# Performance work log

Hardware: AMD Instinct MI355X
Metric: run time of the kernel (lower is better)

## Reference

```python
import jax, jax.numpy as jnp
import numpy as np

N_NODES = 50000
N_EDGES = 800000


def _gcn_conv(x, W, b, src, dst, norm, n_nodes):
    # PyG GCNConv: out = D^{-1/2} (A + I) D^{-1/2} (x W) + b
    h = x @ W                                  # [N, out]
    msg = h[src] * norm[:, None]               # [E+N, out] gathered, normalized messages
    agg = jax.ops.segment_sum(msg, dst, num_segments=n_nodes)
    return agg + b


def _build_norm(edge_index, n_nodes):
    # add self-loops, compute symmetric degree normalization
    loop = jnp.arange(n_nodes, dtype=edge_index.dtype)
    src = jnp.concatenate([edge_index[0], loop])
    dst = jnp.concatenate([edge_index[1], loop])
    deg = jnp.zeros((n_nodes,), jnp.float32).at[dst].add(1.0)
    dinv = jnp.where(deg > 0, jax.lax.rsqrt(deg), 0.0)
    norm = dinv[src] * dinv[dst]
    return src, dst, norm


def setup_inputs() -> dict:
    key = jax.random.key(0)
    ks = jax.random.split(key, 5)
    x = jax.random.normal(ks[0], (N_NODES, 128), dtype=jnp.float32)
    edge_index = jax.random.randint(ks[1], (2, N_EDGES), 0, N_NODES, dtype=jnp.int64)
    s1 = 1.0 / np.sqrt(128)
    s2 = 1.0 / np.sqrt(128)
    s3 = 1.0 / np.sqrt(64)
    return {
        "x": x,
        "edge_index": edge_index,
        "W1": jax.random.normal(ks[2], (128, 128), dtype=jnp.float32) * s1,
        "b1": jnp.zeros((128,), jnp.float32),
        "W2": jax.random.normal(ks[3], (128, 64), dtype=jnp.float32) * s2,
        "b2": jnp.zeros((64,), jnp.float32),
        "W3": jax.random.normal(ks[4], (64, 128), dtype=jnp.float32) * s3,
        "b3": jnp.zeros((128,), jnp.float32),
    }


def reference(x, edge_index, W1, b1, W2, b2, W3, b3):
    n = x.shape[0]
    src, dst, norm = _build_norm(edge_index, n)
    # dropout is identity in eval mode
    h = jax.nn.relu(_gcn_conv(x, W1, b1, src, dst, norm, n))
    h = jax.nn.relu(_gcn_conv(h, W2, b2, src, dst, norm, n))
    out = _gcn_conv(h, W3, b3, src, dst, norm, n)
    return out
```

## Files before the change

### kernel.cpp

```cpp
#include <hip/hip_runtime.h>


#define DEV_INLINE __device__ __forceinline__

typedef unsigned int uint;
typedef unsigned short ushort;
typedef __attribute__((ext_vector_type(8))) short bf16x8;
typedef __attribute__((ext_vector_type(4))) float f32x4;

static DEV_INLINE uint f2bf_rne(float f) {
    uint u = __float_as_uint(f);
    return (u + 0x7FFFu + ((u >> 16) & 1u)) >> 16;
}
static DEV_INLINE uint pack2(float a, float b) { return f2bf_rne(a) | (f2bf_rne(b) << 16); }
static DEV_INLINE float bflo(uint u) { return __uint_as_float(u << 16); }
static DEV_INLINE float bfhi(uint u) { return __uint_as_float(u & 0xFFFF0000u); }

static DEV_INLINE void fma8(float4& a, float4& b, float n, const uint4& v) {
    a.x = fmaf(n, bflo(v.x), a.x); a.y = fmaf(n, bfhi(v.x), a.y);
    a.z = fmaf(n, bflo(v.y), a.z); a.w = fmaf(n, bfhi(v.y), a.w);
    b.x = fmaf(n, bflo(v.z), b.x); b.y = fmaf(n, bfhi(v.z), b.y);
    b.z = fmaf(n, bflo(v.w), b.z); b.w = fmaf(n, bfhi(v.w), b.w);
}

static DEV_INLINE void split8(const float4& x0, const float4& x1, bf16x8& ah, bf16x8& al) {
    float xs[8] = {x0.x, x0.y, x0.z, x0.w, x1.x, x1.y, x1.z, x1.w};
#pragma unroll
    for (int j = 0; j < 8; ++j) {
        uint u = __float_as_uint(xs[j]);
        ah[j] = (short)(u >> 16);
        float r = xs[j] - __uint_as_float(u & 0xFFFF0000u);
        al[j] = (short)(__float_as_uint(r) >> 16);
    }
}


__global__ __launch_bounds__(256) void hist_coarse_kernel(
    const int* __restrict__ dst, int* __restrict__ cnt196, int E, int NBK)
{
    __shared__ int h[256];
    if ((int)threadIdx.x < NBK) h[threadIdx.x] = 0;
    __syncthreads();
    for (int i = blockIdx.x * blockDim.x + threadIdx.x; i < E; i += gridDim.x * blockDim.x)
        atomicAdd(&h[dst[i] >> 8], 1);
    __syncthreads();
    if ((int)threadIdx.x < NBK) {
        int v = h[threadIdx.x];
        if (v) atomicAdd(&cnt196[threadIdx.x], v);
    }
}

__global__ void scan_coarse_kernel(const int* __restrict__ cnt196, int* __restrict__ base196,
                                   int* __restrict__ cursor196, int* __restrict__ rowptr,
                                   int NBK, int N, int E)
{
    __shared__ int buf[256];
    const int tid = threadIdx.x;
    int v = (tid < NBK) ? cnt196[tid] : 0;
    buf[tid] = v;
    __syncthreads();
#pragma unroll
    for (int ofs = 1; ofs < 256; ofs <<= 1) {
        int t = (tid >= ofs) ? buf[tid - ofs] : 0;
        __syncthreads();
        buf[tid] += t;
        __syncthreads();
    }
    if (tid < NBK) {
        int b = buf[tid] - v;
        base196[tid] = b;
        cursor196[tid] = b;
    }
    if (tid == 0) rowptr[N] = E;
}

__global__ __launch_bounds__(256) void scatter_coarse_kernel(
    const int* __restrict__ src, const int* __restrict__ dst,
    int* __restrict__ cursor196, uint* __restrict__ pkg, int E, int NBK)
{
    __shared__ int histL[256];
    __shared__ int baseL[256];
    const int tid = threadIdx.x;
    const int c0  = blockIdx.x * 2048;
    if (tid < NBK) histL[tid] = 0;
    __syncthreads();

    uint mypk[8];
    int  myn = 0;
#pragma unroll
    for (int k = 0; k < 8; ++k) {
        int idx = c0 + k * 256 + tid;
        if (idx < E) {
            uint pk = ((uint)dst[idx] << 16) | (uint)(src[idx] & 0xFFFF);
            mypk[myn++] = pk;
            atomicAdd(&histL[pk >> 24], 1);
        }
    }
    __syncthreads();
    if (tid < NBK) {
        int h = histL[tid];
        baseL[tid] = (h > 0) ? atomicAdd(&cursor196[tid], h) : 0;
        histL[tid] = 0;
    }
    __syncthreads();
    for (int k = 0; k < myn; ++k) {
        uint pk = mypk[k];
        int b = pk >> 24;
        int pos = baseL[b] + atomicAdd(&histL[b], 1);
        pkg[pos] = pk;
    }
}

__global__ __launch_bounds__(256) void build_fine_kernel(
    const uint* __restrict__ pkg, const int* __restrict__ cnt196,
    const int* __restrict__ base196, int* __restrict__ rowptr,
    float* __restrict__ dinv, ushort* __restrict__ perm, int N)
{
    __shared__ uint   pkL[8192];
    __shared__ ushort outS[8192];
    __shared__ int hist[256];
    __shared__ int buf[256];
    const int b   = blockIdx.x;
    const int tid = threadIdx.x;
    const int base = base196[b];
    int nE = cnt196[b];
    if (nE > 8192) nE = 8192;

    hist[tid] = 0;
    __syncthreads();
    for (int i = tid; i < nE; i += 256) {
        uint pk = pkg[base + i];
        pkL[i] = pk;
        atomicAdd(&hist[(pk >> 16) & 255], 1);
    }
    __syncthreads();

    int cnt = hist[tid];
    buf[tid] = cnt;
    __syncthreads();
#pragma unroll
    for (int ofs = 1; ofs < 256; ofs <<= 1) {
        int t = (tid >= ofs) ? buf[tid - ofs] : 0;
        __syncthreads();
        buf[tid] += t;
        __syncthreads();
    }
    int excl = buf[tid] - cnt;
    int node = b * 256 + tid;
    if (node < N) {
        rowptr[node] = base + excl;
        dinv[node]   = rsqrtf((float)(cnt + 1));
    }
    hist[tid] = excl;
    __syncthreads();
    for (int i = tid; i < nE; i += 256) {
        uint pk = pkL[i];
        int d = (pk >> 16) & 255;
        int pos = atomicAdd(&hist[d], 1);
        outS[pos] = (ushort)(pk & 0xFFFFu);
    }
    __syncthreads();
    for (int i = tid; i < nE; i += 256) perm[base + i] = outS[i];
}


template<int K, int NOUT>
static DEV_INLINE void prep_one(const float* __restrict__ W,
                                ushort* __restrict__ Wh, ushort* __restrict__ Wl, int id) {
    constexpr int C = NOUT / 16;
    int lane = id & 63;
    int tc   = id >> 6;
    int c = tc % C, t = tc / C;
    int krow = t * 32 + (lane >> 4) * 8;
    int col  = c * 16 + (lane & 15);
#pragma unroll
    for (int j = 0; j < 8; ++j) {
        float w = W[(size_t)(krow + j) * NOUT + col];
        uint u = __float_as_uint(w);
        Wh[(size_t)id * 8 + j] = (ushort)(u >> 16);
        float r = w - __uint_as_float(u & 0xFFFF0000u);
        Wl[(size_t)id * 8 + j] = (ushort)(__float_as_uint(r) >> 16);
    }
}

__global__ void prep_wfrag_all_kernel(
    const float* __restrict__ W1, const float* __restrict__ W2, const float* __restrict__ W3,
    ushort* w1h, ushort* w1l, ushort* w2h, ushort* w2l, ushort* w3h, ushort* w3l)
{
    int id = blockIdx.x * 256 + threadIdx.x;
    if (id < 2048)       prep_one<128, 128>(W1, w1h, w1l, id);
    else if (id < 3072)  prep_one<128, 64>(W2, w2h, w2l, id - 2048);
    else if (id < 4096)  prep_one<64, 128>(W3, w3h, w3l, id - 3072);
}


template<int K, int NOUT, bool ABF, bool PRE, bool POSTB, bool OUTBF>
__global__ __launch_bounds__(256) void gemm_mfma_kernel(
    const void* __restrict__ A, const ushort* __restrict__ Whf, const ushort* __restrict__ Wlf,
    const float* __restrict__ bias_k, const float* __restrict__ bias_n,
    void* __restrict__ Cout, int N)
{
    constexpr int C  = NOUT / 16;
    constexpr int T  = K / 32;
    const int tid  = threadIdx.x;
    const int w    = tid >> 6;
    const int lane = tid & 63;
    const int row0 = blockIdx.x * 64 + w * 16;

    const int arow  = row0 + (lane & 15);
    const int arowc = (arow < N) ? arow : (N - 1);
    const int lq    = (lane >> 4);

    const bf16x8* WH = reinterpret_cast<const bf16x8*>(Whf);
    const bf16x8* WL = reinterpret_cast<const bf16x8*>(Wlf);

    f32x4 acc[C];
#pragma unroll
    for (int c = 0; c < C; ++c) acc[c] = (f32x4){0.f, 0.f, 0.f, 0.f};

#pragma unroll
    for (int t = 0; t < T; ++t) {
        bf16x8 ah, al;
        if (ABF) {
            const ushort* ap = (const ushort*)A + (size_t)arowc * K + t * 32 + lq * 8;
            ah = *reinterpret_cast<const bf16x8*>(ap);
        } else {
            const float* ap = (const float*)A + (size_t)arowc * K + t * 32 + lq * 8;
            float4 x0 = *reinterpret_cast<const float4*>(ap);
            float4 x1 = *reinterpret_cast<const float4*>(ap + 4);
            if (PRE) {
                const float* bp = bias_k + t * 32 + lq * 8;
                float4 b0 = *reinterpret_cast<const float4*>(bp);
                float4 b1 = *reinterpret_cast<const float4*>(bp + 4);
                x0.x = fmaxf(x0.x + b0.x, 0.f); x0.y = fmaxf(x0.y + b0.y, 0.f);
                x0.z = fmaxf(x0.z + b0.z, 0.f); x0.w = fmaxf(x0.w + b0.w, 0.f);
                x1.x = fmaxf(x1.x + b1.x, 0.f); x1.y = fmaxf(x1.y + b1.y, 0.f);
                x1.z = fmaxf(x1.z + b1.z, 0.f); x1.w = fmaxf(x1.w + b1.w, 0.f);
            }
            split8(x0, x1, ah, al);
        }
#pragma unroll
        for (int c = 0; c < C; ++c) {
            bf16x8 bh = WH[(t * C + c) * 64 + lane];
            bf16x8 bl = WL[(t * C + c) * 64 + lane];
            acc[c] = __builtin_amdgcn_mfma_f32_16x16x32_bf16(ah, bh, acc[c], 0, 0, 0);
            if (!ABF)
                acc[c] = __builtin_amdgcn_mfma_f32_16x16x32_bf16(al, bh, acc[c], 0, 0, 0);
            acc[c] = __builtin_amdgcn_mfma_f32_16x16x32_bf16(ah, bl, acc[c], 0, 0, 0);
        }
    }

    const int rbase = (lane >> 4) * 4;
    const int ccol  = (lane & 15);
#pragma unroll
    for (int c = 0; c < C; ++c) {
        int col = c * 16 + ccol;
        float pb = POSTB ? bias_n[col] : 0.f;
#pragma unroll
        for (int r = 0; r < 4; ++r) {
            int row = row0 + rbase + r;
            if (row < N) {
                float v = acc[c][r] + pb;
                if (OUTBF) ((ushort*)Cout)[(size_t)row * NOUT + col] = (ushort)f2bf_rne(v);
                else       ((float*)Cout)[(size_t)row * NOUT + col] = v;
            }
        }
    }
}


template<int F, bool BIAS, bool RELU, bool OUTBF>
__global__ __launch_bounds__(256) void agg_gather_kernel(
    const uint* __restrict__ H, const int* __restrict__ rowptr,
    const ushort* __restrict__ perm_src, const float* __restrict__ dinv,
    const float* __restrict__ bias, void* __restrict__ OUT, int N)
{
    constexpr int GROUP = F / 8;
    constexpr int FW    = F / 2;
    constexpr int NPB   = 256 / GROUP;
    const int lane = threadIdx.x % GROUP;
    const int g    = threadIdx.x / GROUP;
    const int node = blockIdx.x * NPB + g;
    if (node >= N) return;

    const int beg = rowptr[node];
    const int end = rowptr[node + 1];
    const float di = dinv[node];

    float4 aA = make_float4(0.f, 0.f, 0.f, 0.f), aB = aA;
    float4 bA = aA, bB = aA;
    {
        uint4 v = reinterpret_cast<const uint4*>(H + (size_t)node * FW)[lane];
        fma8(aA, aB, di * di, v);
    }

    int e = beg;
    for (; e + 3 < end; e += 4) {
        int s0 = perm_src[e];     int s1 = perm_src[e + 1];
        int s2 = perm_src[e + 2]; int s3 = perm_src[e + 3];
        float n0 = dinv[s0] * di, n1 = dinv[s1] * di;
        float n2 = dinv[s2] * di, n3 = dinv[s3] * di;
        uint4 v0 = reinterpret_cast<const uint4*>(H + (size_t)s0 * FW)[lane];
        uint4 v1 = reinterpret_cast<const uint4*>(H + (size_t)s1 * FW)[lane];
        uint4 v2 = reinterpret_cast<const uint4*>(H + (size_t)s2 * FW)[lane];
        uint4 v3 = reinterpret_cast<const uint4*>(H + (size_t)s3 * FW)[lane];
        fma8(aA, aB, n0, v0);
        fma8(bA, bB, n1, v1);
        fma8(aA, aB, n2, v2);
        fma8(bA, bB, n3, v3);
    }
    for (; e < end; ++e) {
        int s0 = perm_src[e];
        float n0 = dinv[s0] * di;
        uint4 v0 = reinterpret_cast<const uint4*>(H + (size_t)s0 * FW)[lane];
        fma8(aA, aB, n0, v0);
    }
    aA.x += bA.x; aA.y += bA.y; aA.z += bA.z; aA.w += bA.w;
    aB.x += bB.x; aB.y += bB.y; aB.z += bB.z; aB.w += bB.w;

    if (BIAS) {
        const float4* b4 = reinterpret_cast<const float4*>(bias);
        float4 c0 = b4[lane * 2], c1 = b4[lane * 2 + 1];
        aA.x += c0.x; aA.y += c0.y; aA.z += c0.z; aA.w += c0.w;
        aB.x += c1.x; aB.y += c1.y; aB.z += c1.z; aB.w += c1.w;
    }
    if (RELU) {
        aA.x = fmaxf(aA.x, 0.f); aA.y = fmaxf(aA.y, 0.f);
        aA.z = fmaxf(aA.z, 0.f); aA.w = fmaxf(aA.w, 0.f);
        aB.x = fmaxf(aB.x, 0.f); aB.y = fmaxf(aB.y, 0.f);
        aB.z = fmaxf(aB.z, 0.f); aB.w = fmaxf(aB.w, 0.f);
    }

    if (OUTBF) {
        uint4 u;
        u.x = pack2(aA.x, aA.y); u.y = pack2(aA.z, aA.w);
        u.z = pack2(aB.x, aB.y); u.w = pack2(aB.z, aB.w);
        reinterpret_cast<uint4*>((uint*)OUT + (size_t)node * FW)[lane] = u;
    } else {
        float4* O = reinterpret_cast<float4*>((float*)OUT + (size_t)node * F);
        O[lane * 2]     = aA;
        O[lane * 2 + 1] = aB;
    }
}


static inline size_t align_up(size_t v, size_t a) { return (v + a - 1) / a * a; }

extern "C" void kernel_launch(void* const* d_in, const int* in_sizes, int n_in,
                              void* d_out, int out_size, void* d_ws, size_t ws_size,
                              hipStream_t stream) {
    const float* x  = (const float*)d_in[0];
    const int*   ei = (const int*)d_in[1];
    const float* W1 = (const float*)d_in[2];
    const float* b1 = (const float*)d_in[3];
    const float* W2 = (const float*)d_in[4];
    const float* b2 = (const float*)d_in[5];
    const float* W3 = (const float*)d_in[6];
    const float* b3 = (const float*)d_in[7];
    float* out = (float*)d_out;

    const int N = in_sizes[0] / 128;
    const int E = in_sizes[1] / 2;
    const int* src = ei;
    const int* dst = ei + E;
    const int NBK = (N + 255) / 256;

    char* ws = (char*)d_ws;
    size_t off = 0;
    float* dinv   = (float*)(ws + off); off = align_up(off + (size_t)N * 4, 512);
    int*   rowptr = (int*)  (ws + off); off = align_up(off + (size_t)(N + 1) * 4, 512);
    int*   cnt196    = (int*)(ws + off); off = align_up(off + (size_t)NBK * 4, 512);
    int*   base196   = (int*)(ws + off); off = align_up(off + (size_t)NBK * 4, 512);
    int*   cursor196 = (int*)(ws + off); off = align_up(off + (size_t)NBK * 4, 512);
    ushort* perm_src = (ushort*)(ws + off); off = align_up(off + (size_t)E * 2, 512);
    uint*  pkg    = (uint*) (ws + off); off = align_up(off + (size_t)E * 4, 512);
    uint*  Hbf    = (uint*) (ws + off); off = align_up(off + (size_t)N * 128 * 2, 512);
    char*  Ashare = (char*) (ws + off); off = align_up(off + (size_t)N * 128 * 4, 512);
    ushort* w1h   = (ushort*)(ws + off); off = align_up(off + (size_t)128 * 128 * 2, 512);
    ushort* w1l   = (ushort*)(ws + off); off = align_up(off + (size_t)128 * 128 * 2, 512);
    ushort* w2h   = (ushort*)(ws + off); off = align_up(off + (size_t)128 * 64 * 2, 512);
    ushort* w2l   = (ushort*)(ws + off); off = align_up(off + (size_t)128 * 64 * 2, 512);
    ushort* w3h   = (ushort*)(ws + off); off = align_up(off + (size_t)64 * 128 * 2, 512);
    ushort* w3l   = (ushort*)(ws + off); off = align_up(off + (size_t)64 * 128 * 2, 512);
    (void)ws_size;

    uint* H1bf   = Hbf;
    uint* H2bf   = Hbf;
    uint* H3bf   = Hbf + (size_t)N * 32;
    uint* AGG1bf = (uint*)Ashare;
    float* T     = (float*)Ashare;

    const int TPB = 256;
    dim3 blk(TPB);
    int gRow = (N + 63) / 64;

    prep_wfrag_all_kernel<<<16, blk, 0, stream>>>(W1, W2, W3, w1h, w1l, w2h, w2l, w3h, w3l);

    hipMemsetAsync(cnt196, 0, (size_t)NBK * 4, stream);
    hist_coarse_kernel<<<392, blk, 0, stream>>>(dst, cnt196, E, NBK);
    scan_coarse_kernel<<<1, blk, 0, stream>>>(cnt196, base196, cursor196, rowptr, NBK, N, E);
    scatter_coarse_kernel<<<(E + 2047) / 2048, blk, 0, stream>>>(src, dst, cursor196, pkg, E, NBK);
    build_fine_kernel<<<NBK, blk, 0, stream>>>(pkg, cnt196, base196, rowptr, dinv, perm_src, N);

    gemm_mfma_kernel<128, 128, false, false, false, true><<<gRow, blk, 0, stream>>>(
        x, w1h, w1l, nullptr, nullptr, H1bf, N);
    agg_gather_kernel<128, true, true, true><<<(N + 15) / 16, blk, 0, stream>>>(
        H1bf, rowptr, perm_src, dinv, b1, AGG1bf, N);

    gemm_mfma_kernel<128, 64, true, false, false, true><<<gRow, blk, 0, stream>>>(
        AGG1bf, w2h, w2l, nullptr, nullptr, H2bf, N);
    agg_gather_kernel<64, true, true, true><<<(N + 31) / 32, blk, 0, stream>>>(
        H2bf, rowptr, perm_src, dinv, b2, H3bf, N);

    agg_gather_kernel<64, false, false, false><<<(N + 31) / 32, blk, 0, stream>>>(
        H3bf, rowptr, perm_src, dinv, nullptr, T, N);
    gemm_mfma_kernel<64, 128, false, false, true, false><<<gRow, blk, 0, stream>>>(
        T, w3h, w3l, nullptr, b3, out, N);
}
```

Baseline: 229.6 us.

## Fold dinv into GEMM outputs and fuse aggregation with following GEMMs

Pre-scales each GEMM output row by dinv[src] so the gather no longer loads dinv per neighbour; the aggregation becomes a plain sum and is scaled by dinv[dst] afterwards. The layer-1 aggregation is fused with the layer-2 GEMM, and the layer-3 aggregation with the layer-3 GEMM, through an LDS tile, so the float/bf16 intermediates no longer make a round trip through global memory. The scatter kernel re-reads src and dst instead of holding the packed values in registers. This cuts kernel launches and intermediate traffic, at the cost of a gather-phase load imbalance inside each fused block and a changed rounding order.

```diff
diff --git a/kernel.cpp b/kernel.cpp
--- a/kernel.cpp
+++ b/kernel.cpp
@@ -12,15 +12,14 @@
     uint u = __float_as_uint(f);
     return (u + 0x7FFFu + ((u >> 16) & 1u)) >> 16;
 }
-static DEV_INLINE uint pack2(float a, float b) { return f2bf_rne(a) | (f2bf_rne(b) << 16); }
 static DEV_INLINE float bflo(uint u) { return __uint_as_float(u << 16); }
 static DEV_INLINE float bfhi(uint u) { return __uint_as_float(u & 0xFFFF0000u); }
 
-static DEV_INLINE void fma8(float4& a, float4& b, float n, const uint4& v) {
-    a.x = fmaf(n, bflo(v.x), a.x); a.y = fmaf(n, bfhi(v.x), a.y);
-    a.z = fmaf(n, bflo(v.y), a.z); a.w = fmaf(n, bfhi(v.y), a.w);
-    b.x = fmaf(n, bflo(v.z), b.x); b.y = fmaf(n, bfhi(v.z), b.y);
-    b.z = fmaf(n, bflo(v.w), b.z); b.w = fmaf(n, bfhi(v.w), b.w);
+static DEV_INLINE void add8(float4& a, float4& b, const uint4& v) {
+    a.x += bflo(v.x); a.y += bfhi(v.x);
+    a.z += bflo(v.y); a.w += bfhi(v.y);
+    b.x += bflo(v.z); b.y += bfhi(v.z);
+    b.z += bflo(v.w); b.w += bfhi(v.w);
 }
 
 static DEV_INLINE void split8(const float4& x0, const float4& x1, bf16x8& ah, bf16x8& al) {
@@ -34,6 +33,40 @@
     }
 }
 
+template<int FW>
+static DEV_INLINE void gather_sum(const uint* __restrict__ H, const ushort* __restrict__ perm,
+                                  int beg, int end, int lane, float4& o0, float4& o1)
+{
+    float4 A0 = o0, A1 = o1;
+    float4 B0 = make_float4(0.f,0.f,0.f,0.f), B1 = B0, C0 = B0, C1 = B0, D0 = B0, D1 = B0;
+    const uint4* Hv = reinterpret_cast<const uint4*>(H);
+    int e = beg;
+    for (; e + 8 <= end; e += 8) {
+        int s0 = perm[e];     int s1 = perm[e + 1];
+        int s2 = perm[e + 2]; int s3 = perm[e + 3];
+        int s4 = perm[e + 4]; int s5 = perm[e + 5];
+        int s6 = perm[e + 6]; int s7 = perm[e + 7];
+        uint4 v0 = Hv[(size_t)s0 * (FW / 4) + lane];
+        uint4 v1 = Hv[(size_t)s1 * (FW / 4) + lane];
+        uint4 v2 = Hv[(size_t)s2 * (FW / 4) + lane];
+        uint4 v3 = Hv[(size_t)s3 * (FW / 4) + lane];
+        uint4 v4 = Hv[(size_t)s4 * (FW / 4) + lane];
+        uint4 v5 = Hv[(size_t)s5 * (FW / 4) + lane];
+        uint4 v6 = Hv[(size_t)s6 * (FW / 4) + lane];
+        uint4 v7 = Hv[(size_t)s7 * (FW / 4) + lane];
+        add8(A0, A1, v0); add8(B0, B1, v1); add8(C0, C1, v2); add8(D0, D1, v3);
+        add8(A0, A1, v4); add8(B0, B1, v5); add8(C0, C1, v6); add8(D0, D1, v7);
+    }
+    for (; e < end; ++e) {
+        uint4 v = Hv[(size_t)perm[e] * (FW / 4) + lane];
+        add8(A0, A1, v);
+    }
+    o0.x = A0.x + B0.x + C0.x + D0.x; o0.y = A0.y + B0.y + C0.y + D0.y;
+    o0.z = A0.z + B0.z + C0.z + D0.z; o0.w = A0.w + B0.w + C0.w + D0.w;
+    o1.x = A1.x + B1.x + C1.x + D1.x; o1.y = A1.y + B1.y + C1.y + D1.y;
+    o1.z = A1.z + B1.z + C1.z + D1.z; o1.w = A1.w + B1.w + C1.w + D1.w;
+}
+
 
 __global__ __launch_bounds__(256) void hist_coarse_kernel(
     const int* __restrict__ dst, int* __restrict__ cnt196, int E, int NBK)
@@ -84,17 +117,10 @@
     const int c0  = blockIdx.x * 2048;
     if (tid < NBK) histL[tid] = 0;
     __syncthreads();
-
-    uint mypk[8];
-    int  myn = 0;
 #pragma unroll
     for (int k = 0; k < 8; ++k) {
         int idx = c0 + k * 256 + tid;
-        if (idx < E) {
-            uint pk = ((uint)dst[idx] << 16) | (uint)(src[idx] & 0xFFFF);
-            mypk[myn++] = pk;
-            atomicAdd(&histL[pk >> 24], 1);
-        }
+        if (idx < E) atomicAdd(&histL[dst[idx] >> 8], 1);
     }
     __syncthreads();
     if (tid < NBK) {
@@ -103,11 +129,15 @@
         histL[tid] = 0;
     }
     __syncthreads();
-    for (int k = 0; k < myn; ++k) {
-        uint pk = mypk[k];
-        int b = pk >> 24;
-        int pos = baseL[b] + atomicAdd(&histL[b], 1);
-        pkg[pos] = pk;
+#pragma unroll
+    for (int k = 0; k < 8; ++k) {
+        int idx = c0 + k * 256 + tid;
+        if (idx < E) {
+            int d = dst[idx];
+            int b = d >> 8;
+            int pos = baseL[b] + atomicAdd(&histL[b], 1);
+            pkg[pos] = ((uint)d << 16) | (uint)(src[idx] & 0xFFFF);
+        }
     }
 }
 
@@ -194,19 +224,15 @@
 }
 
 
-template<int K, int NOUT, bool ABF, bool PRE, bool POSTB, bool OUTBF>
-__global__ __launch_bounds__(256) void gemm_mfma_kernel(
-    const void* __restrict__ A, const ushort* __restrict__ Whf, const ushort* __restrict__ Wlf,
-    const float* __restrict__ bias_k, const float* __restrict__ bias_n,
-    void* __restrict__ Cout, int N)
-{
-    constexpr int C  = NOUT / 16;
-    constexpr int T  = K / 32;
+__global__ __launch_bounds__(256) void gemm1_kernel(
+    const float* __restrict__ A, const ushort* __restrict__ Whf, const ushort* __restrict__ Wlf,
+    const float* __restrict__ dinv, ushort* __restrict__ Cout, int N)
+{
+    constexpr int C = 8, T = 4, K = 128, NOUT = 128;
     const int tid  = threadIdx.x;
     const int w    = tid >> 6;
     const int lane = tid & 63;
     const int row0 = blockIdx.x * 64 + w * 16;
-
     const int arow  = row0 + (lane & 15);
     const int arowc = (arow < N) ? arow : (N - 1);
     const int lq    = (lane >> 4);
@@ -220,32 +246,17 @@
 
 #pragma unroll
     for (int t = 0; t < T; ++t) {
+        const float* ap = A + (size_t)arowc * K + t * 32 + lq * 8;
+        float4 x0 = *reinterpret_cast<const float4*>(ap);
+        float4 x1 = *reinterpret_cast<const float4*>(ap + 4);
         bf16x8 ah, al;
-        if (ABF) {
-            const ushort* ap = (const ushort*)A + (size_t)arowc * K + t * 32 + lq * 8;
-            ah = *reinterpret_cast<const bf16x8*>(ap);
-        } else {
-            const float* ap = (const float*)A + (size_t)arowc * K + t * 32 + lq * 8;
-            float4 x0 = *reinterpret_cast<const float4*>(ap);
-            float4 x1 = *reinterpret_cast<const float4*>(ap + 4);
-            if (PRE) {
-                const float* bp = bias_k + t * 32 + lq * 8;
-                float4 b0 = *reinterpret_cast<const float4*>(bp);
-                float4 b1 = *reinterpret_cast<const float4*>(bp + 4);
-                x0.x = fmaxf(x0.x + b0.x, 0.f); x0.y = fmaxf(x0.y + b0.y, 0.f);
-                x0.z = fmaxf(x0.z + b0.z, 0.f); x0.w = fmaxf(x0.w + b0.w, 0.f);
-                x1.x = fmaxf(x1.x + b1.x, 0.f); x1.y = fmaxf(x1.y + b1.y, 0.f);
-                x1.z = fmaxf(x1.z + b1.z, 0.f); x1.w = fmaxf(x1.w + b1.w, 0.f);
-            }
-            split8(x0, x1, ah, al);
-        }
+        split8(x0, x1, ah, al);
 #pragma unroll
         for (int c = 0; c < C; ++c) {
             bf16x8 bh = WH[(t * C + c) * 64 + lane];
             bf16x8 bl = WL[(t * C + c) * 64 + lane];
             acc[c] = __builtin_amdgcn_mfma_f32_16x16x32_bf16(ah, bh, acc[c], 0, 0, 0);
-            if (!ABF)
-                acc[c] = __builtin_amdgcn_mfma_f32_16x16x32_bf16(al, bh, acc[c], 0, 0, 0);
+            acc[c] = __builtin_amdgcn_mfma_f32_16x16x32_bf16(al, bh, acc[c], 0, 0, 0);
             acc[c] = __builtin_amdgcn_mfma_f32_16x16x32_bf16(ah, bl, acc[c], 0, 0, 0);
         }
     }
@@ -253,31 +264,111 @@
     const int rbase = (lane >> 4) * 4;
     const int ccol  = (lane & 15);
 #pragma unroll
-    for (int c = 0; c < C; ++c) {
-        int col = c * 16 + ccol;
-        float pb = POSTB ? bias_n[col] : 0.f;
-#pragma unroll
-        for (int r = 0; r < 4; ++r) {
-            int row = row0 + rbase + r;
-            if (row < N) {
-                float v = acc[c][r] + pb;
-                if (OUTBF) ((ushort*)Cout)[(size_t)row * NOUT + col] = (ushort)f2bf_rne(v);
-                else       ((float*)Cout)[(size_t)row * NOUT + col] = v;
+    for (int r = 0; r < 4; ++r) {
+        int row = row0 + rbase + r;
+        if (row < N) {
+            float di = dinv[row];
+#pragma unroll
+            for (int c = 0; c < C; ++c) {
+                int col = c * 16 + ccol;
+                Cout[(size_t)row * NOUT + col] = (ushort)f2bf_rne(acc[c][r] * di);
             }
         }
     }
 }
 
 
-template<int F, bool BIAS, bool RELU, bool OUTBF>
-__global__ __launch_bounds__(256) void agg_gather_kernel(
+__global__ __launch_bounds__(256) void fused_agg1_gemm2_kernel(
+    const uint* __restrict__ H1, const int* __restrict__ rowptr,
+    const ushort* __restrict__ perm, const float* __restrict__ dinv,
+    const float* __restrict__ b1, const ushort* __restrict__ w2h,
+    const ushort* __restrict__ w2l, ushort* __restrict__ H2, int N)
+{
+    __shared__ float As[64][132];
+    const int tid  = threadIdx.x;
+    const int row0 = blockIdx.x * 64;
+
+    {
+        const int lg = tid & 15;
+        const int g  = tid >> 4;
+        const float4* b4 = reinterpret_cast<const float4*>(b1);
+        float4 bb0 = b4[lg * 2], bb1 = b4[lg * 2 + 1];
+#pragma unroll
+        for (int p = 0; p < 4; ++p) {
+            int nl = p * 16 + g;
+            int node = row0 + nl;
+            int nodec = (node < N) ? node : (N - 1);
+            int beg = rowptr[nodec], end = rowptr[nodec + 1];
+            float di = dinv[nodec];
+            float4 o0 = make_float4(0.f,0.f,0.f,0.f), o1 = o0;
+            uint4 sv = reinterpret_cast<const uint4*>(H1 + (size_t)nodec * 64)[lg];
+            add8(o0, o1, sv);
+            gather_sum<64>(H1, perm, beg, end, lg, o0, o1);
+            float4 r0, r1;
+            r0.x = fmaxf(fmaf(di, o0.x, bb0.x), 0.f);
+            r0.y = fmaxf(fmaf(di, o0.y, bb0.y), 0.f);
+            r0.z = fmaxf(fmaf(di, o0.z, bb0.z), 0.f);
+            r0.w = fmaxf(fmaf(di, o0.w, bb0.w), 0.f);
+            r1.x = fmaxf(fmaf(di, o1.x, bb1.x), 0.f);
+            r1.y = fmaxf(fmaf(di, o1.y, bb1.y), 0.f);
+            r1.z = fmaxf(fmaf(di, o1.z, bb1.z), 0.f);
+            r1.w = fmaxf(fmaf(di, o1.w, bb1.w), 0.f);
+            *reinterpret_cast<float4*>(&As[nl][lg * 8])     = r0;
+            *reinterpret_cast<float4*>(&As[nl][lg * 8 + 4]) = r1;
+        }
+    }
+    __syncthreads();
+
+    const int w    = tid >> 6;
+    const int lane = tid & 63;
+    const int ar   = w * 16 + (lane & 15);
+    const int lq   = lane >> 4;
+    const bf16x8* WH = reinterpret_cast<const bf16x8*>(w2h);
+    const bf16x8* WL = reinterpret_cast<const bf16x8*>(w2l);
+
+    f32x4 acc[4];
+#pragma unroll
+    for (int c = 0; c < 4; ++c) acc[c] = (f32x4){0.f, 0.f, 0.f, 0.f};
+
+#pragma unroll
+    for (int t = 0; t < 4; ++t) {
+        float4 x0 = *reinterpret_cast<const float4*>(&As[ar][t * 32 + lq * 8]);
+        float4 x1 = *reinterpret_cast<const float4*>(&As[ar][t * 32 + lq * 8 + 4]);
+        bf16x8 ah, al;
+        split8(x0, x1, ah, al);
+#pragma unroll
+        for (int c = 0; c < 4; ++c) {
+            bf16x8 bh = WH[(t * 4 + c) * 64 + lane];
+            bf16x8 bl = WL[(t * 4 + c) * 64 + lane];
+            acc[c] = __builtin_amdgcn_mfma_f32_16x16x32_bf16(ah, bh, acc[c], 0, 0, 0);
+            acc[c] = __builtin_amdgcn_mfma_f32_16x16x32_bf16(al, bh, acc[c], 0, 0, 0);
+            acc[c] = __builtin_amdgcn_mfma_f32_16x16x32_bf16(ah, bl, acc[c], 0, 0, 0);
+        }
+    }
+
+    const int rbase = (lane >> 4) * 4;
+    const int ccol  = (lane & 15);
+#pragma unroll
+    for (int r = 0; r < 4; ++r) {
+        int grow = row0 + w * 16 + rbase + r;
+        if (grow < N) {
+            float di = dinv[grow];
+#pragma unroll
+            for (int c = 0; c < 4; ++c) {
+                int col = c * 16 + ccol;
+                H2[(size_t)grow * 64 + col] = (ushort)f2bf_rne(acc[c][r] * di);
+            }
+        }
+    }
+}
+
+
+__global__ __launch_bounds__(256) void gather2_kernel(
     const uint* __restrict__ H, const int* __restrict__ rowptr,
-    const ushort* __restrict__ perm_src, const float* __restrict__ dinv,
-    const float* __restrict__ bias, void* __restrict__ OUT, int N)
-{
-    constexpr int GROUP = F / 8;
-    constexpr int FW    = F / 2;
-    constexpr int NPB   = 256 / GROUP;
+    const ushort* __restrict__ perm, const float* __restrict__ dinv,
+    const float* __restrict__ bias, ushort* __restrict__ OUT, int N)
+{
+    constexpr int GROUP = 8, FW = 32, NPB = 32;
     const int lane = threadIdx.x % GROUP;
     const int g    = threadIdx.x / GROUP;
     const int node = blockIdx.x * NPB + g;
@@ -287,59 +378,103 @@
     const int end = rowptr[node + 1];
     const float di = dinv[node];
 
-    float4 aA = make_float4(0.f, 0.f, 0.f, 0.f), aB = aA;
-    float4 bA = aA, bB = aA;
+    float4 o0 = make_float4(0.f,0.f,0.f,0.f), o1 = o0;
+    uint4 sv = reinterpret_cast<const uint4*>(H + (size_t)node * FW)[lane];
+    add8(o0, o1, sv);
+    gather_sum<FW>(H, perm, beg, end, lane, o0, o1);
+
+    const float4* b4 = reinterpret_cast<const float4*>(bias);
+    float4 c0 = b4[lane * 2], c1 = b4[lane * 2 + 1];
+    float v[8];
+    v[0] = fmaxf(fmaf(di, o0.x, c0.x), 0.f) * di;
+    v[1] = fmaxf(fmaf(di, o0.y, c0.y), 0.f) * di;
+    v[2] = fmaxf(fmaf(di, o0.z, c0.z), 0.f) * di;
+    v[3] = fmaxf(fmaf(di, o0.w, c0.w), 0.f) * di;
+    v[4] = fmaxf(fmaf(di, o1.x, c1.x), 0.f) * di;
+    v[5] = fmaxf(fmaf(di, o1.y, c1.y), 0.f) * di;
+    v[6] = fmaxf(fmaf(di, o1.z, c1.z), 0.f) * di;
+    v[7] = fmaxf(fmaf(di, o1.w, c1.w), 0.f) * di;
+    uint4 u;
+    u.x = f2bf_rne(v[0]) | (f2bf_rne(v[1]) << 16);
+    u.y = f2bf_rne(v[2]) | (f2bf_rne(v[3]) << 16);
+    u.z = f2bf_rne(v[4]) | (f2bf_rne(v[5]) << 16);
+    u.w = f2bf_rne(v[6]) | (f2bf_rne(v[7]) << 16);
+    reinterpret_cast<uint4*>(OUT + (size_t)node * 64)[lane] = u;
+}
+
+
+__global__ __launch_bounds__(256) void fused_agg3_gemm3_kernel(
+    const uint* __restrict__ H3, const int* __restrict__ rowptr,
+    const ushort* __restrict__ perm, const float* __restrict__ dinv,
+    const ushort* __restrict__ w3h, const ushort* __restrict__ w3l,
+    const float* __restrict__ b3, float* __restrict__ out, int N)
+{
+    __shared__ float Ts[64][68];
+    const int tid  = threadIdx.x;
+    const int row0 = blockIdx.x * 64;
+
     {
-        uint4 v = reinterpret_cast<const uint4*>(H + (size_t)node * FW)[lane];
-        fma8(aA, aB, di * di, v);
-    }
-
-    int e = beg;
-    for (; e + 3 < end; e += 4) {
-        int s0 = perm_src[e];     int s1 = perm_src[e + 1];
-        int s2 = perm_src[e + 2]; int s3 = perm_src[e + 3];
-        float n0 = dinv[s0] * di, n1 = dinv[s1] * di;
-        float n2 = dinv[s2] * di, n3 = dinv[s3] * di;
-        uint4 v0 = reinterpret_cast<const uint4*>(H + (size_t)s0 * FW)[lane];
-        uint4 v1 = reinterpret_cast<const uint4*>(H + (size_t)s1 * FW)[lane];
-        uint4 v2 = reinterpret_cast<const uint4*>(H + (size_t)s2 * FW)[lane];
-        uint4 v3 = reinterpret_cast<const uint4*>(H + (size_t)s3 * FW)[lane];
-        fma8(aA, aB, n0, v0);
-        fma8(bA, bB, n1, v1);
-        fma8(aA, aB, n2, v2);
-        fma8(bA, bB, n3, v3);
-    }
-    for (; e < end; ++e) {
-        int s0 = perm_src[e];
-        float n0 = dinv[s0] * di;
-        uint4 v0 = reinterpret_cast<const uint4*>(H + (size_t)s0 * FW)[lane];
-        fma8(aA, aB, n0, v0);
-    }
-    aA.x += bA.x; aA.y += bA.y; aA.z += bA.z; aA.w += bA.w;
-    aB.x += bB.x; aB.y += bB.y; aB.z += bB.z; aB.w += bB.w;
-
-    if (BIAS) {
-        const float4* b4 = reinterpret_cast<const float4*>(bias);
-        float4 c0 = b4[lane * 2], c1 = b4[lane * 2 + 1];
-        aA.x += c0.x; aA.y += c0.y; aA.z += c0.z; aA.w += c0.w;
-        aB.x += c1.x; aB.y += c1.y; aB.z += c1.z; aB.w += c1.w;
-    }
-    if (RELU) {
-        aA.x = fmaxf(aA.x, 0.f); aA.y = fmaxf(aA.y, 0.f);
-        aA.z = fmaxf(aA.z, 0.f); aA.w = fmaxf(aA.w, 0.f);
-        aB.x = fmaxf(aB.x, 0.f); aB.y = fmaxf(aB.y, 0.f);
-        aB.z = fmaxf(aB.z, 0.f); aB.w = fmaxf(aB.w, 0.f);
-    }
-
-    if (OUTBF) {
-        uint4 u;
-        u.x = pack2(aA.x, aA.y); u.y = pack2(aA.z, aA.w);
-        u.z = pack2(aB.x, aB.y); u.w = pack2(aB.z, aB.w);
-        reinterpret_cast<uint4*>((uint*)OUT + (size_t)node * FW)[lane] = u;
-    } else {
-        float4* O = reinterpret_cast<float4*>((float*)OUT + (size_t)node * F);
-        O[lane * 2]     = aA;
-        O[lane * 2 + 1] = aB;
+        const int lg = tid & 7;
+        const int g  = tid >> 3;
+#pragma unroll
+        for (int p = 0; p < 2; ++p) {
+            int nl = p * 32 + g;
+            int node = row0 + nl;
+            int nodec = (node < N) ? node : (N - 1);
+            int beg = rowptr[nodec], end = rowptr[nodec + 1];
+            float di = dinv[nodec];
+            float4 o0 = make_float4(0.f,0.f,0.f,0.f), o1 = o0;
+            uint4 sv = reinterpret_cast<const uint4*>(H3 + (size_t)nodec * 32)[lg];
+            add8(o0, o1, sv);
+            gather_sum<32>(H3, perm, beg, end, lg, o0, o1);
+            float4 r0, r1;
+            r0.x = di * o0.x; r0.y = di * o0.y; r0.z = di * o0.z; r0.w = di * o0.w;
+            r1.x = di * o1.x; r1.y = di * o1.y; r1.z = di * o1.z; r1.w = di * o1.w;
+            *reinterpret_cast<float4*>(&Ts[nl][lg * 8])     = r0;
+            *reinterpret_cast<float4*>(&Ts[nl][lg * 8 + 4]) = r1;
+        }
+    }
+    __syncthreads();
+
+    const int w    = tid >> 6;
+    const int lane = tid & 63;
+    const int ar   = w * 16 + (lane & 15);
+    const int lq   = lane >> 4;
+    const bf16x8* WH = reinterpret_cast<const bf16x8*>(w3h);
+    const bf16x8* WL = reinterpret_cast<const bf16x8*>(w3l);
+
+    f32x4 acc[8];
+#pragma unroll
+    for (int c = 0; c < 8; ++c) acc[c] = (f32x4){0.f, 0.f, 0.f, 0.f};
+
+#pragma unroll
+    for (int t = 0; t < 2; ++t) {
+        float4 x0 = *reinterpret_cast<const float4*>(&Ts[ar][t * 32 + lq * 8]);
+        float4 x1 = *reinterpret_cast<const float4*>(&Ts[ar][t * 32 + lq * 8 + 4]);
+        bf16x8 ah, al;
+        split8(x0, x1, ah, al);
+#pragma unroll
+        for (int c = 0; c < 8; ++c) {
+            bf16x8 bh = WH[(t * 8 + c) * 64 + lane];
+            bf16x8 bl = WL[(t * 8 + c) * 64 + lane];
+            acc[c] = __builtin_amdgcn_mfma_f32_16x16x32_bf16(ah, bh, acc[c], 0, 0, 0);
+            acc[c] = __builtin_amdgcn_mfma_f32_16x16x32_bf16(al, bh, acc[c], 0, 0, 0);
+            acc[c] = __builtin_amdgcn_mfma_f32_16x16x32_bf16(ah, bl, acc[c], 0, 0, 0);
+        }
+    }
+
+    const int rbase = (lane >> 4) * 4;
+    const int ccol  = (lane & 15);
+#pragma unroll
+    for (int r = 0; r < 4; ++r) {
+        int grow = row0 + w * 16 + rbase + r;
+        if (grow < N) {
+#pragma unroll
+            for (int c = 0; c < 8; ++c) {
+                int col = c * 16 + ccol;
+                out[(size_t)grow * 128 + col] = acc[c][r] + b3[col];
+            }
+        }
     }
 }
 
@@ -367,28 +502,23 @@
 
     char* ws = (char*)d_ws;
     size_t off = 0;
-    float* dinv   = (float*)(ws + off); off = align_up(off + (size_t)N * 4, 512);
-    int*   rowptr = (int*)  (ws + off); off = align_up(off + (size_t)(N + 1) * 4, 512);
-    int*   cnt196    = (int*)(ws + off); off = align_up(off + (size_t)NBK * 4, 512);
-    int*   base196   = (int*)(ws + off); off = align_up(off + (size_t)NBK * 4, 512);
-    int*   cursor196 = (int*)(ws + off); off = align_up(off + (size_t)NBK * 4, 512);
-    ushort* perm_src = (ushort*)(ws + off); off = align_up(off + (size_t)E * 2, 512);
-    uint*  pkg    = (uint*) (ws + off); off = align_up(off + (size_t)E * 4, 512);
-    uint*  Hbf    = (uint*) (ws + off); off = align_up(off + (size_t)N * 128 * 2, 512);
-    char*  Ashare = (char*) (ws + off); off = align_up(off + (size_t)N * 128 * 4, 512);
-    ushort* w1h   = (ushort*)(ws + off); off = align_up(off + (size_t)128 * 128 * 2, 512);
-    ushort* w1l   = (ushort*)(ws + off); off = align_up(off + (size_t)128 * 128 * 2, 512);
-    ushort* w2h   = (ushort*)(ws + off); off = align_up(off + (size_t)128 * 64 * 2, 512);
-    ushort* w2l   = (ushort*)(ws + off); off = align_up(off + (size_t)128 * 64 * 2, 512);
-    ushort* w3h   = (ushort*)(ws + off); off = align_up(off + (size_t)64 * 128 * 2, 512);
-    ushort* w3l   = (ushort*)(ws + off); off = align_up(off + (size_t)64 * 128 * 2, 512);
+    float* dinv      = (float*)(ws + off); off = align_up(off + (size_t)N * 4, 512);
+    int*   rowptr    = (int*)  (ws + off); off = align_up(off + (size_t)(N + 1) * 4, 512);
+    int*   cnt196    = (int*)  (ws + off); off = align_up(off + (size_t)NBK * 4, 512);
+    int*   base196   = (int*)  (ws + off); off = align_up(off + (size_t)NBK * 4, 512);
+    int*   cursor196 = (int*)  (ws + off); off = align_up(off + (size_t)NBK * 4, 512);
+    ushort* perm     = (ushort*)(ws + off); off = align_up(off + (size_t)E * 2, 512);
+    uint*  pkg       = (uint*) (ws + off); off = align_up(off + (size_t)E * 4, 512);
+    uint*  H1bf      = (uint*) (ws + off); off = align_up(off + (size_t)N * 64 * 4, 512);
+    uint*  H2bf      = (uint*) (ws + off); off = align_up(off + (size_t)N * 32 * 4, 512);
+    uint*  H3bf      = (uint*) (ws + off); off = align_up(off + (size_t)N * 32 * 4, 512);
+    ushort* w1h = (ushort*)(ws + off); off = align_up(off + (size_t)128 * 128 * 2, 512);
+    ushort* w1l = (ushort*)(ws + off); off = align_up(off + (size_t)128 * 128 * 2, 512);
+    ushort* w2h = (ushort*)(ws + off); off = align_up(off + (size_t)128 * 64 * 2, 512);
+    ushort* w2l = (ushort*)(ws + off); off = align_up(off + (size_t)128 * 64 * 2, 512);
+    ushort* w3h = (ushort*)(ws + off); off = align_up(off + (size_t)64 * 128 * 2, 512);
+    ushort* w3l = (ushort*)(ws + off); off = align_up(off + (size_t)64 * 128 * 2, 512);
     (void)ws_size;
-
-    uint* H1bf   = Hbf;
-    uint* H2bf   = Hbf;
-    uint* H3bf   = Hbf + (size_t)N * 32;
-    uint* AGG1bf = (uint*)Ashare;
-    float* T     = (float*)Ashare;
 
     const int TPB = 256;
     dim3 blk(TPB);
@@ -400,20 +530,13 @@
     hist_coarse_kernel<<<392, blk, 0, stream>>>(dst, cnt196, E, NBK);
     scan_coarse_kernel<<<1, blk, 0, stream>>>(cnt196, base196, cursor196, rowptr, NBK, N, E);
     scatter_coarse_kernel<<<(E + 2047) / 2048, blk, 0, stream>>>(src, dst, cursor196, pkg, E, NBK);
-    build_fine_kernel<<<NBK, blk, 0, stream>>>(pkg, cnt196, base196, rowptr, dinv, perm_src, N);
-
-    gemm_mfma_kernel<128, 128, false, false, false, true><<<gRow, blk, 0, stream>>>(
-        x, w1h, w1l, nullptr, nullptr, H1bf, N);
-    agg_gather_kernel<128, true, true, true><<<(N + 15) / 16, blk, 0, stream>>>(
-        H1bf, rowptr, perm_src, dinv, b1, AGG1bf, N);
-
-    gemm_mfma_kernel<128, 64, true, false, false, true><<<gRow, blk, 0, stream>>>(
-        AGG1bf, w2h, w2l, nullptr, nullptr, H2bf, N);
-    agg_gather_kernel<64, true, true, true><<<(N + 31) / 32, blk, 0, stream>>>(
-        H2bf, rowptr, perm_src, dinv, b2, H3bf, N);
-
-    agg_gather_kernel<64, false, false, false><<<(N + 31) / 32, blk, 0, stream>>>(
-        H3bf, rowptr, perm_src, dinv, nullptr, T, N);
-    gemm_mfma_kernel<64, 128, false, false, true, false><<<gRow, blk, 0, stream>>>(
-        T, w3h, w3l, nullptr, b3, out, N);
-}
+    build_fine_kernel<<<NBK, blk, 0, stream>>>(pkg, cnt196, base196, rowptr, dinv, perm, N);
+
+    gemm1_kernel<<<gRow, blk, 0, stream>>>(x, w1h, w1l, dinv, (ushort*)H1bf, N);
+    fused_agg1_gemm2_kernel<<<gRow, blk, 0, stream>>>(
+        H1bf, rowptr, perm, dinv, b1, w2h, w2l, (ushort*)H2bf, N);
+    gather2_kernel<<<(N + 31) / 32, blk, 0, stream>>>(
+        H2bf, rowptr, perm, dinv, b2, (ushort*)H3bf, N);
+    fused_agg3_gemm3_kernel<<<gRow, blk, 0, stream>>>(
+        H3bf, rowptr, perm, dinv, w3h, w3l, b3, out, N);
+}
```

Result: slower. 240.5 us (+4.8%).

## Fold symmetric degree normalization into GEMM epilogues and use unweighted gather sums

Applied to the files above, without the earlier changes.

Each GEMM output row is now pre-scaled by dinv[row], and each gather post-scales by dinv[node], so the edge loop becomes a plain sum of bf16 rows with no per-edge dinv lookups or multiplies. The gather loop is unrolled to 8 edges with four independent accumulators to raise memory-level parallelism. The coarse scatter kernel now re-reads src/dst instead of holding packed values in a per-thread register array. The extra rounding of pre-scaled bf16 values slightly changes numerics.

```diff
diff --git a/kernel.cpp b/kernel.cpp
--- a/kernel.cpp
+++ b/kernel.cpp
@@ -12,15 +12,14 @@
     uint u = __float_as_uint(f);
     return (u + 0x7FFFu + ((u >> 16) & 1u)) >> 16;
 }
-static DEV_INLINE uint pack2(float a, float b) { return f2bf_rne(a) | (f2bf_rne(b) << 16); }
 static DEV_INLINE float bflo(uint u) { return __uint_as_float(u << 16); }
 static DEV_INLINE float bfhi(uint u) { return __uint_as_float(u & 0xFFFF0000u); }
 
-static DEV_INLINE void fma8(float4& a, float4& b, float n, const uint4& v) {
-    a.x = fmaf(n, bflo(v.x), a.x); a.y = fmaf(n, bfhi(v.x), a.y);
-    a.z = fmaf(n, bflo(v.y), a.z); a.w = fmaf(n, bfhi(v.y), a.w);
-    b.x = fmaf(n, bflo(v.z), b.x); b.y = fmaf(n, bfhi(v.z), b.y);
-    b.z = fmaf(n, bflo(v.w), b.z); b.w = fmaf(n, bfhi(v.w), b.w);
+static DEV_INLINE void add8(float4& a, float4& b, const uint4& v) {
+    a.x += bflo(v.x); a.y += bfhi(v.x);
+    a.z += bflo(v.y); a.w += bfhi(v.y);
+    b.x += bflo(v.z); b.y += bfhi(v.z);
+    b.z += bflo(v.w); b.w += bfhi(v.w);
 }
 
 static DEV_INLINE void split8(const float4& x0, const float4& x1, bf16x8& ah, bf16x8& al) {
@@ -34,6 +33,40 @@
     }
 }
 
+template<int FW>
+static DEV_INLINE void gather_sum(const uint* __restrict__ H, const ushort* __restrict__ perm,
+                                  int beg, int end, int lane, float4& o0, float4& o1)
+{
+    float4 A0 = o0, A1 = o1;
+    float4 B0 = make_float4(0.f,0.f,0.f,0.f), B1 = B0, C0 = B0, C1 = B0, D0 = B0, D1 = B0;
+    const uint4* Hv = reinterpret_cast<const uint4*>(H);
+    int e = beg;
+    for (; e + 8 <= end; e += 8) {
+        int s0 = perm[e];     int s1 = perm[e + 1];
+        int s2 = perm[e + 2]; int s3 = perm[e + 3];
+        int s4 = perm[e + 4]; int s5 = perm[e + 5];
+        int s6 = perm[e + 6]; int s7 = perm[e + 7];
+        uint4 v0 = Hv[(size_t)s0 * (FW / 4) + lane];
+        uint4 v1 = Hv[(size_t)s1 * (FW / 4) + lane];
+        uint4 v2 = Hv[(size_t)s2 * (FW / 4) + lane];
+        uint4 v3 = Hv[(size_t)s3 * (FW / 4) + lane];
+        uint4 v4 = Hv[(size_t)s4 * (FW / 4) + lane];
+        uint4 v5 = Hv[(size_t)s5 * (FW / 4) + lane];
+        uint4 v6 = Hv[(size_t)s6 * (FW / 4) + lane];
+        uint4 v7 = Hv[(size_t)s7 * (FW / 4) + lane];
+        add8(A0, A1, v0); add8(B0, B1, v1); add8(C0, C1, v2); add8(D0, D1, v3);
+        add8(A0, A1, v4); add8(B0, B1, v5); add8(C0, C1, v6); add8(D0, D1, v7);
+    }
+    for (; e < end; ++e) {
+        uint4 v = Hv[(size_t)perm[e] * (FW / 4) + lane];
+        add8(A0, A1, v);
+    }
+    o0.x = A0.x + B0.x + C0.x + D0.x; o0.y = A0.y + B0.y + C0.y + D0.y;
+    o0.z = A0.z + B0.z + C0.z + D0.z; o0.w = A0.w + B0.w + C0.w + D0.w;
+    o1.x = A1.x + B1.x + C1.x + D1.x; o1.y = A1.y + B1.y + C1.y + D1.y;
+    o1.z = A1.z + B1.z + C1.z + D1.z; o1.w = A1.w + B1.w + C1.w + D1.w;
+}
+
 
 __global__ __launch_bounds__(256) void hist_coarse_kernel(
     const int* __restrict__ dst, int* __restrict__ cnt196, int E, int NBK)
@@ -84,17 +117,10 @@
     const int c0  = blockIdx.x * 2048;
     if (tid < NBK) histL[tid] = 0;
     __syncthreads();
-
-    uint mypk[8];
-    int  myn = 0;
 #pragma unroll
     for (int k = 0; k < 8; ++k) {
         int idx = c0 + k * 256 + tid;
-        if (idx < E) {
-            uint pk = ((uint)dst[idx] << 16) | (uint)(src[idx] & 0xFFFF);
-            mypk[myn++] = pk;
-            atomicAdd(&histL[pk >> 24], 1);
-        }
+        if (idx < E) atomicAdd(&histL[dst[idx] >> 8], 1);
     }
     __syncthreads();
     if (tid < NBK) {
@@ -103,11 +129,15 @@
         histL[tid] = 0;
     }
     __syncthreads();
-    for (int k = 0; k < myn; ++k) {
-        uint pk = mypk[k];
-        int b = pk >> 24;
-        int pos = baseL[b] + atomicAdd(&histL[b], 1);
-        pkg[pos] = pk;
+#pragma unroll
+    for (int k = 0; k < 8; ++k) {
+        int idx = c0 + k * 256 + tid;
+        if (idx < E) {
+            int d = dst[idx];
+            int b = d >> 8;
+            int pos = baseL[b] + atomicAdd(&histL[b], 1);
+            pkg[pos] = ((uint)d << 16) | (uint)(src[idx] & 0xFFFF);
+        }
     }
 }
 
@@ -194,10 +224,10 @@
 }
 
 
-template<int K, int NOUT, bool ABF, bool PRE, bool POSTB, bool OUTBF>
+template<int K, int NOUT, bool ABF, bool SCALEDI, bool POSTB, bool OUTBF>
 __global__ __launch_bounds__(256) void gemm_mfma_kernel(
     const void* __restrict__ A, const ushort* __restrict__ Whf, const ushort* __restrict__ Wlf,
-    const float* __restrict__ bias_k, const float* __restrict__ bias_n,
+    const float* __restrict__ dinv, const float* __restrict__ bias_n,
     void* __restrict__ Cout, int N)
 {
     constexpr int C  = NOUT / 16;
@@ -228,15 +258,6 @@
             const float* ap = (const float*)A + (size_t)arowc * K + t * 32 + lq * 8;
             float4 x0 = *reinterpret_cast<const float4*>(ap);
             float4 x1 = *reinterpret_cast<const float4*>(ap + 4);
-            if (PRE) {
-                const float* bp = bias_k + t * 32 + lq * 8;
-                float4 b0 = *reinterpret_cast<const float4*>(bp);
-                float4 b1 = *reinterpret_cast<const float4*>(bp + 4);
-                x0.x = fmaxf(x0.x + b0.x, 0.f); x0.y = fmaxf(x0.y + b0.y, 0.f);
-                x0.z = fmaxf(x0.z + b0.z, 0.f); x0.w = fmaxf(x0.w + b0.w, 0.f);
-                x1.x = fmaxf(x1.x + b1.x, 0.f); x1.y = fmaxf(x1.y + b1.y, 0.f);
-                x1.z = fmaxf(x1.z + b1.z, 0.f); x1.w = fmaxf(x1.w + b1.w, 0.f);
-            }
             split8(x0, x1, ah, al);
         }
 #pragma unroll
@@ -253,14 +274,16 @@
     const int rbase = (lane >> 4) * 4;
     const int ccol  = (lane & 15);
 #pragma unroll
-    for (int c = 0; c < C; ++c) {
-        int col = c * 16 + ccol;
-        float pb = POSTB ? bias_n[col] : 0.f;
-#pragma unroll
-        for (int r = 0; r < 4; ++r) {
-            int row = row0 + rbase + r;
-            if (row < N) {
-                float v = acc[c][r] + pb;
+    for (int r = 0; r < 4; ++r) {
+        int row = row0 + rbase + r;
+        if (row < N) {
+            float di = SCALEDI ? dinv[row] : 1.0f;
+#pragma unroll
+            for (int c = 0; c < C; ++c) {
+                int col = c * 16 + ccol;
+                float v = acc[c][r];
+                if (SCALEDI) v *= di;
+                if (POSTB)   v += bias_n[col];
                 if (OUTBF) ((ushort*)Cout)[(size_t)row * NOUT + col] = (ushort)f2bf_rne(v);
                 else       ((float*)Cout)[(size_t)row * NOUT + col] = v;
             }
@@ -269,14 +292,13 @@
 }
 
 
-template<int F, bool BIAS, bool RELU, bool OUTBF>
-__global__ __launch_bounds__(256) void agg_gather_kernel(
+template<int FW, bool RELU, bool POSTDI, bool OUTBF>
+__global__ __launch_bounds__(256) void gather_kernel(
     const uint* __restrict__ H, const int* __restrict__ rowptr,
-    const ushort* __restrict__ perm_src, const float* __restrict__ dinv,
+    const ushort* __restrict__ perm, const float* __restrict__ dinv,
     const float* __restrict__ bias, void* __restrict__ OUT, int N)
 {
-    constexpr int GROUP = F / 8;
-    constexpr int FW    = F / 2;
+    constexpr int GROUP = FW / 4;
     constexpr int NPB   = 256 / GROUP;
     const int lane = threadIdx.x % GROUP;
     const int g    = threadIdx.x / GROUP;
@@ -287,59 +309,35 @@
     const int end = rowptr[node + 1];
     const float di = dinv[node];
 
-    float4 aA = make_float4(0.f, 0.f, 0.f, 0.f), aB = aA;
-    float4 bA = aA, bB = aA;
-    {
-        uint4 v = reinterpret_cast<const uint4*>(H + (size_t)node * FW)[lane];
-        fma8(aA, aB, di * di, v);
-    }
-
-    int e = beg;
-    for (; e + 3 < end; e += 4) {
-        int s0 = perm_src[e];     int s1 = perm_src[e + 1];
-        int s2 = perm_src[e + 2]; int s3 = perm_src[e + 3];
-        float n0 = dinv[s0] * di, n1 = dinv[s1] * di;
-        float n2 = dinv[s2] * di, n3 = dinv[s3] * di;
-        uint4 v0 = reinterpret_cast<const uint4*>(H + (size_t)s0 * FW)[lane];
-        uint4 v1 = reinterpret_cast<const uint4*>(H + (size_t)s1 * FW)[lane];
-        uint4 v2 = reinterpret_cast<const uint4*>(H + (size_t)s2 * FW)[lane];
-        uint4 v3 = reinterpret_cast<const uint4*>(H + (size_t)s3 * FW)[lane];
-        fma8(aA, aB, n0, v0);
-        fma8(bA, bB, n1, v1);
-        fma8(aA, aB, n2, v2);
-        fma8(bA, bB, n3, v3);
-    }
-    for (; e < end; ++e) {
-        int s0 = perm_src[e];
-        float n0 = dinv[s0] * di;
-        uint4 v0 = reinterpret_cast<const uint4*>(H + (size_t)s0 * FW)[lane];
-        fma8(aA, aB, n0, v0);
-    }
-    aA.x += bA.x; aA.y += bA.y; aA.z += bA.z; aA.w += bA.w;
-    aB.x += bB.x; aB.y += bB.y; aB.z += bB.z; aB.w += bB.w;
-
-    if (BIAS) {
-        const float4* b4 = reinterpret_cast<const float4*>(bias);
-        float4 c0 = b4[lane * 2], c1 = b4[lane * 2 + 1];
-        aA.x += c0.x; aA.y += c0.y; aA.z += c0.z; aA.w += c0.w;
-        aB.x += c1.x; aB.y += c1.y; aB.z += c1.z; aB.w += c1.w;
-    }
+    float4 o0 = make_float4(0.f,0.f,0.f,0.f), o1 = o0;
+    uint4 sv = reinterpret_cast<const uint4*>(H + (size_t)node * FW)[lane];
+    add8(o0, o1, sv);
+    gather_sum<FW>(H, perm, beg, end, lane, o0, o1);
+
+    float v[8] = {o0.x, o0.y, o0.z, o0.w, o1.x, o1.y, o1.z, o1.w};
+#pragma unroll
+    for (int j = 0; j < 8; ++j) v[j] *= di;
     if (RELU) {
-        aA.x = fmaxf(aA.x, 0.f); aA.y = fmaxf(aA.y, 0.f);
-        aA.z = fmaxf(aA.z, 0.f); aA.w = fmaxf(aA.w, 0.f);
-        aB.x = fmaxf(aB.x, 0.f); aB.y = fmaxf(aB.y, 0.f);
-        aB.z = fmaxf(aB.z, 0.f); aB.w = fmaxf(aB.w, 0.f);
+        const float* bp = bias + lane * 8;
+#pragma unroll
+        for (int j = 0; j < 8; ++j) v[j] = fmaxf(v[j] + bp[j], 0.f);
+    }
+    if (POSTDI) {
+#pragma unroll
+        for (int j = 0; j < 8; ++j) v[j] *= di;
     }
 
     if (OUTBF) {
         uint4 u;
-        u.x = pack2(aA.x, aA.y); u.y = pack2(aA.z, aA.w);
-        u.z = pack2(aB.x, aB.y); u.w = pack2(aB.z, aB.w);
+        u.x = f2bf_rne(v[0]) | (f2bf_rne(v[1]) << 16);
+        u.y = f2bf_rne(v[2]) | (f2bf_rne(v[3]) << 16);
+        u.z = f2bf_rne(v[4]) | (f2bf_rne(v[5]) << 16);
+        u.w = f2bf_rne(v[6]) | (f2bf_rne(v[7]) << 16);
         reinterpret_cast<uint4*>((uint*)OUT + (size_t)node * FW)[lane] = u;
     } else {
-        float4* O = reinterpret_cast<float4*>((float*)OUT + (size_t)node * F);
-        O[lane * 2]     = aA;
-        O[lane * 2 + 1] = aB;
+        float4* O = reinterpret_cast<float4*>((float*)OUT + (size_t)node * (FW * 2));
+        O[lane * 2]     = make_float4(v[0], v[1], v[2], v[3]);
+        O[lane * 2 + 1] = make_float4(v[4], v[5], v[6], v[7]);
     }
 }
 
@@ -367,28 +365,28 @@
 
     char* ws = (char*)d_ws;
     size_t off = 0;
-    float* dinv   = (float*)(ws + off); off = align_up(off + (size_t)N * 4, 512);
-    int*   rowptr = (int*)  (ws + off); off = align_up(off + (size_t)(N + 1) * 4, 512);
-    int*   cnt196    = (int*)(ws + off); off = align_up(off + (size_t)NBK * 4, 512);
-    int*   base196   = (int*)(ws + off); off = align_up(off + (size_t)NBK * 4, 512);
-    int*   cursor196 = (int*)(ws + off); off = align_up(off + (size_t)NBK * 4, 512);
-    ushort* perm_src = (ushort*)(ws + off); off = align_up(off + (size_t)E * 2, 512);
-    uint*  pkg    = (uint*) (ws + off); off = align_up(off + (size_t)E * 4, 512);
-    uint*  Hbf    = (uint*) (ws + off); off = align_up(off + (size_t)N * 128 * 2, 512);
-    char*  Ashare = (char*) (ws + off); off = align_up(off + (size_t)N * 128 * 4, 512);
-    ushort* w1h   = (ushort*)(ws + off); off = align_up(off + (size_t)128 * 128 * 2, 512);
-    ushort* w1l   = (ushort*)(ws + off); off = align_up(off + (size_t)128 * 128 * 2, 512);
-    ushort* w2h   = (ushort*)(ws + off); off = align_up(off + (size_t)128 * 64 * 2, 512);
-    ushort* w2l   = (ushort*)(ws + off); off = align_up(off + (size_t)128 * 64 * 2, 512);
-    ushort* w3h   = (ushort*)(ws + off); off = align_up(off + (size_t)64 * 128 * 2, 512);
-    ushort* w3l   = (ushort*)(ws + off); off = align_up(off + (size_t)64 * 128 * 2, 512);
+    float* dinv      = (float*)(ws + off); off = align_up(off + (size_t)N * 4, 512);
+    int*   rowptr    = (int*)  (ws + off); off = align_up(off + (size_t)(N + 1) * 4, 512);
+    int*   cnt196    = (int*)  (ws + off); off = align_up(off + (size_t)NBK * 4, 512);
+    int*   base196   = (int*)  (ws + off); off = align_up(off + (size_t)NBK * 4, 512);
+    int*   cursor196 = (int*)  (ws + off); off = align_up(off + (size_t)NBK * 4, 512);
+    ushort* perm     = (ushort*)(ws + off); off = align_up(off + (size_t)E * 2, 512);
+    uint*  pkg       = (uint*) (ws + off); off = align_up(off + (size_t)E * 4, 512);
+    uint*  regA      = (uint*) (ws + off); off = align_up(off + (size_t)N * 64 * 4, 512);
+    uint*  regB      = (uint*) (ws + off); off = align_up(off + (size_t)N * 64 * 4, 512);
+    ushort* w1h = (ushort*)(ws + off); off = align_up(off + (size_t)128 * 128 * 2, 512);
+    ushort* w1l = (ushort*)(ws + off); off = align_up(off + (size_t)128 * 128 * 2, 512);
+    ushort* w2h = (ushort*)(ws + off); off = align_up(off + (size_t)128 * 64 * 2, 512);
+    ushort* w2l = (ushort*)(ws + off); off = align_up(off + (size_t)128 * 64 * 2, 512);
+    ushort* w3h = (ushort*)(ws + off); off = align_up(off + (size_t)64 * 128 * 2, 512);
+    ushort* w3l = (ushort*)(ws + off); off = align_up(off + (size_t)64 * 128 * 2, 512);
     (void)ws_size;
 
-    uint* H1bf   = Hbf;
-    uint* H2bf   = Hbf;
-    uint* H3bf   = Hbf + (size_t)N * 32;
-    uint* AGG1bf = (uint*)Ashare;
-    float* T     = (float*)Ashare;
+    uint*  H1bf  = regA;
+    uint*  AGG1  = regB;
+    uint*  H2bf  = regA;
+    uint*  H3bf  = regA + (size_t)N * 32;
+    float* T     = (float*)regB;
 
     const int TPB = 256;
     dim3 blk(TPB);
@@ -400,20 +398,18 @@
     hist_coarse_kernel<<<392, blk, 0, stream>>>(dst, cnt196, E, NBK);
     scan_coarse_kernel<<<1, blk, 0, stream>>>(cnt196, base196, cursor196, rowptr, NBK, N, E);
     scatter_coarse_kernel<<<(E + 2047) / 2048, blk, 0, stream>>>(src, dst, cursor196, pkg, E, NBK);
-    build_fine_kernel<<<NBK, blk, 0, stream>>>(pkg, cnt196, base196, rowptr, dinv, perm_src, N);
-
-    gemm_mfma_kernel<128, 128, false, false, false, true><<<gRow, blk, 0, stream>>>(
-        x, w1h, w1l, nullptr, nullptr, H1bf, N);
-    agg_gather_kernel<128, true, true, true><<<(N + 15) / 16, blk, 0, stream>>>(
-        H1bf, rowptr, perm_src, dinv, b1, AGG1bf, N);
-
-    gemm_mfma_kernel<128, 64, true, false, false, true><<<gRow, blk, 0, stream>>>(
-        AGG1bf, w2h, w2l, nullptr, nullptr, H2bf, N);
-    agg_gather_kernel<64, true, true, true><<<(N + 31) / 32, blk, 0, stream>>>(
-        H2bf, rowptr, perm_src, dinv, b2, H3bf, N);
-
-    agg_gather_kernel<64, false, false, false><<<(N + 31) / 32, blk, 0, stream>>>(
-        H3bf, rowptr, perm_src, dinv, nullptr, T, N);
+    build_fine_kernel<<<NBK, blk, 0, stream>>>(pkg, cnt196, base196, rowptr, dinv, perm, N);
+
+    gemm_mfma_kernel<128, 128, false, true, false, true><<<gRow, blk, 0, stream>>>(
+        x, w1h, w1l, dinv, nullptr, H1bf, N);
+    gather_kernel<64, true, false, true><<<(N + 15) / 16, blk, 0, stream>>>(
+        H1bf, rowptr, perm, dinv, b1, AGG1, N);
+    gemm_mfma_kernel<128, 64, true, true, false, true><<<gRow, blk, 0, stream>>>(
+        AGG1, w2h, w2l, dinv, nullptr, H2bf, N);
+    gather_kernel<32, true, true, true><<<(N + 31) / 32, blk, 0, stream>>>(
+        H2bf, rowptr, perm, dinv, b2, H3bf, N);
+    gather_kernel<32, false, false, false><<<(N + 31) / 32, blk, 0, stream>>>(
+        H3bf, rowptr, perm, dinv, nullptr, T, N);
     gemm_mfma_kernel<64, 128, false, false, true, false><<<gRow, blk, 0, stream>>>(
         T, w3h, w3l, nullptr, b3, out, N);
 }
```

New measurement: 238.5 us. 3.9% more time.
